# Kernel tuning notes

Hardware: AMD Instinct MI355X
Metric: run time of the kernel (lower is better)

Reference implementation:

```python
import jax, jax.numpy as jnp
import numpy as np

D = 128          # embedding_size
K = 1024         # num_embedding
DECAY = 0.99
EPS = 1e-5
VQ_COMMIT = 0.25
B, T = 16, 4096


def setup_inputs() -> dict:
    key = jax.random.key(0)
    k1, k2, k3 = jax.random.split(key, 3)
    emb = jax.random.normal(k2, (D, K), dtype=jnp.float32)
    return {
        "input": jax.random.normal(k1, (B, T, D), dtype=jnp.float32),
        "embedding": emb,
        "cluster_size": jnp.zeros((K,), dtype=jnp.float32),
        "embedding_mean": emb.copy(),
    }


def reference(input, embedding, cluster_size, embedding_mean):
    # ---- quantize: squared-distance argmin over codebook ----
    flatten = input.reshape(-1, D)                                   # [N, D]
    dist = ((flatten ** 2).sum(1, keepdims=True)
            - 2.0 * flatten @ embedding
            + (embedding ** 2).sum(0, keepdims=True))                # [N, K]
    embedding_ind = jnp.argmin(dist, axis=1)                         # [N]
    code = embedding_ind.reshape(input.shape[:-1])                   # [B, T]

    # ---- dequantize: codebook gather ----
    quantize = jnp.take(embedding.T, code, axis=0)                   # [B, T, D]

    # ---- EMA codebook update (training mode) ----
    N = flatten.shape[0]
    counts = jax.ops.segment_sum(jnp.ones((N,), input.dtype), embedding_ind,
                                 num_segments=K)                     # [K]
    emb_sum = jax.ops.segment_sum(flatten, embedding_ind,
                                  num_segments=K).T                  # [D, K]
    new_cluster_size = cluster_size * DECAY + (1.0 - DECAY) * counts
    new_embedding_mean = embedding_mean * DECAY + (1.0 - DECAY) * emb_sum
    n = new_cluster_size.sum()
    cs = (new_cluster_size + EPS) / (n + K * EPS) * n
    new_embedding = new_embedding_mean / cs[None, :]                 # [D, K]

    # ---- straight-through estimator + commitment loss ----
    quantize_st = input + jax.lax.stop_gradient(quantize - input)
    diff = VQ_COMMIT * jnp.mean(
        (jax.lax.stop_gradient(quantize_st) - input) ** 2)

    return (quantize_st, diff, code,
            new_embedding, new_cluster_size, new_embedding_mean)
```

## Files before the change

kernel.cpp:

```cpp
#include <hip/hip_runtime.h>
#include <hip/hip_fp16.h>
#include <math.h>

#define D_ 128
#define K_ 1024
#define N_ 65536
#define DECAY_ 0.99f
#define OMD_ 0.01f
#define EPS_ 1e-5f
#define VQC_ 0.25f
#define M1_ 0.14f
#define M2_ 0.14f
#define BIAS_ 96.0f
#define CLMIN_ 0.5f
#define CLMAX_ 508.0f
#define WSEG 32

typedef __attribute__((ext_vector_type(8))) _Float16 half8;
typedef __attribute__((ext_vector_type(4))) float f32x4;

#define WOFF_CODE  0
#define WOFF_E2    65536
#define WOFF_CNT   66560
#define WOFF_SSQ   67584
#define WOFF_RCNT  67585
#define WOFF_BASE  67648
#define WOFF_CURS  68736
#define WOFF_ORDER 69760
#define WOFF_ET    136320
#define WOFF_PART  267392
#define WOFF_CSORT 398464
#define WOFF_RLIST 791680
#define WOFF_EF    857216

#define OOFF_Q     0
#define OOFF_DIFF  8388608
#define OOFF_CODE  8388609
#define OOFF_NEMB  8454145
#define OOFF_NCS   8585217
#define OOFF_NMEAN 8586241

__device__ __forceinline__ unsigned umin32(unsigned a, unsigned b) { return a < b ? a : b; }
__device__ __forceinline__ unsigned umax32(unsigned a, unsigned b) { return a > b ? a : b; }

__device__ __forceinline__ void gld16(const unsigned short* g, unsigned short* l) {
    __builtin_amdgcn_global_load_lds(
        (const __attribute__((address_space(1))) unsigned int*)g,
        (__attribute__((address_space(3))) unsigned int*)l, 16, 0, 0);
}

__launch_bounds__(256)
__global__ void k_prep(const float* __restrict__ E, float* __restrict__ Et,
                       unsigned short* __restrict__ Ef, float* __restrict__ e2,
                       int* __restrict__ cnt, float* __restrict__ part1) {
    __shared__ float tile[128 * 17];
    __shared__ float e2s[16];
    int tid = threadIdx.x;
    int b = blockIdx.x;
    int c0 = b * 16;
    if (b == 0) {
        for (int i = tid; i < 1026; i += 256) cnt[i] = 0;
    }
    #pragma unroll
    for (int i = 0; i < 8; ++i) part1[b * 2048 + i * 256 + tid] = 0.f;
    if (tid < 16) e2s[tid] = 0.f;
    #pragma unroll
    for (int i = 0; i < 8; ++i) {
        int idx = i * 256 + tid;
        int d = idx >> 4, cc = idx & 15;
        tile[d * 17 + cc] = E[d * K_ + c0 + cc];
    }
    __syncthreads();
    #pragma unroll
    for (int i = 0; i < 8; ++i) {
        int idx = i * 256 + tid;
        int cc = idx >> 7, d = idx & 127;
        Et[(size_t)(c0 + cc) * D_ + d] = tile[d * 17 + cc];
    }
    int L = tid & 63, s = tid >> 6;
    int cc = L & 15;
    int d0 = s * 32 + ((L >> 4) << 3);
    unsigned short h[8];
    float sq = 0.f;
    #pragma unroll
    for (int j = 0; j < 8; ++j) {
        float e = tile[(d0 + j) * 17 + cc];
        sq = fmaf(e, e, sq);
        h[j] = __half_as_ushort(__float2half(-2.f * e));
    }
    int T = b * 256 + tid;
    #pragma unroll
    for (int j = 0; j < 8; ++j) Ef[T * 8 + j] = h[j];
    atomicAdd(&e2s[cc], sq);
    __syncthreads();
    if (tid < 16) e2[c0 + tid] = e2s[tid];
}

__launch_bounds__(512, 4)
__global__ void k_argmin_mfma(const float* __restrict__ x, const unsigned short* __restrict__ Ef,
                              const float* __restrict__ e2,
                              int* __restrict__ code_i, float* __restrict__ code_f,
                              int* __restrict__ cnt, int* __restrict__ rcnt,
                              int* __restrict__ rlist, const float* __restrict__ Et) {
    __shared__ unsigned short Bs[3][8192];
    __shared__ float e2s[K_];
    int tid = threadIdx.x;
    int w = tid >> 6, L = tid & 63, quad = L >> 4, col = L & 15;
    int mg = w >> 1, ng = w & 1;
    int n0 = blockIdx.x * 128;

    for (int i = tid; i < K_; i += 512) e2s[i] = e2[i];

    half8 ah[2][4];
    #pragma unroll
    for (int mt = 0; mt < 2; ++mt) {
        int tok = n0 + (2 * mg + mt) * 16 + col;
        #pragma unroll
        for (int s = 0; s < 4; ++s) {
            const float* p = x + (size_t)tok * D_ + s * 32 + quad * 8;
            float4 u0 = *(const float4*)(p);
            float4 u1 = *(const float4*)(p + 4);
            ah[mt][s][0] = (_Float16)u0.x; ah[mt][s][1] = (_Float16)u0.y;
            ah[mt][s][2] = (_Float16)u0.z; ah[mt][s][3] = (_Float16)u0.w;
            ah[mt][s][4] = (_Float16)u1.x; ah[mt][s][5] = (_Float16)u1.y;
            ah[mt][s][6] = (_Float16)u1.z; ah[mt][s][7] = (_Float16)u1.w;
        }
    }

    unsigned k1[2][4], k2[2][4], k3[2][4];
    #pragma unroll
    for (int mt = 0; mt < 2; ++mt)
        #pragma unroll
        for (int r = 0; r < 4; ++r) {
            k1[mt][r] = 0xFFFFFFFFu; k2[mt][r] = 0xFFFFFFFFu; k3[mt][r] = 0xFFFFFFFFu;
        }

    __syncthreads();

    #pragma unroll
    for (int i = 0; i < 2; ++i) {
        int o = (w * 2 + i) * 512;
        gld16(Ef + o + L * 8, &Bs[0][o]);
    }
    #pragma unroll
    for (int i = 0; i < 2; ++i) {
        int o = (w * 2 + i) * 512;
        gld16(Ef + 8192 + o + L * 8, &Bs[1][o]);
    }

    #pragma unroll
    for (int q = 0; q < 16; ++q) {
        if (q < 15) asm volatile("s_waitcnt vmcnt(2)" ::: "memory");
        else        asm volatile("s_waitcnt vmcnt(0)" ::: "memory");
        __builtin_amdgcn_s_barrier();
        asm volatile("" ::: "memory");

        const unsigned short* Bp = &Bs[q % 3][0];

        float evb[2];
        #pragma unroll
        for (int nn = 0; nn < 2; ++nn)
            evb[nn] = e2s[q * 64 + (2 * ng + nn) * 16 + col] + BIAS_;
        f32x4 acc[2][2];
        #pragma unroll
        for (int mt = 0; mt < 2; ++mt)
            #pragma unroll
            for (int nn = 0; nn < 2; ++nn)
                #pragma unroll
                for (int r = 0; r < 4; ++r)
                    acc[mt][nn][r] = evb[nn];

        #pragma unroll
        for (int s = 0; s < 4; ++s) {
            half8 bh[2];
            #pragma unroll
            for (int nn = 0; nn < 2; ++nn) {
                int off = (((2 * ng + nn) * 4 + s) * 64 + L) * 8;
                bh[nn] = *(const half8*)(Bp + off);
            }
            #pragma unroll
            for (int nn = 0; nn < 2; ++nn)
                #pragma unroll
                for (int mt = 0; mt < 2; ++mt)
                    acc[mt][nn] = __builtin_amdgcn_mfma_f32_16x16x32_f16(ah[mt][s], bh[nn], acc[mt][nn], 0, 0, 0);
        }

        #pragma unroll
        for (int nn = 0; nn < 2; ++nn) {
            unsigned cb = (unsigned)(q * 64 + (2 * ng + nn) * 16 + col);
            #pragma unroll
            for (int mt = 0; mt < 2; ++mt)
                #pragma unroll
                for (int r = 0; r < 4; ++r) {
                    float dc = fminf(fmaxf(acc[mt][nn][r], CLMIN_), CLMAX_);
                    unsigned key = (__float_as_uint(dc) & 0xFFFFFC00u) | cb;
                    unsigned m1 = umax32(k1[mt][r], key);
                    k1[mt][r]   = umin32(k1[mt][r], key);
                    unsigned m2 = umax32(k2[mt][r], m1);
                    k2[mt][r]   = umin32(k2[mt][r], m1);
                    k3[mt][r]   = umin32(k3[mt][r], m2);
                }
        }

        if (q < 14) {
            const unsigned short* src = Ef + (q + 2) * 8192;
            int sl = (q + 2) % 3;
            #pragma unroll
            for (int i = 0; i < 2; ++i) {
                int o = (w * 2 + i) * 512;
                gld16(src + o + L * 8, &Bs[sl][o]);
            }
        }
    }

    __syncthreads();
    unsigned* mk1 = (unsigned*)&Bs[0][0];
    unsigned* mk2 = mk1 + 256;
    unsigned* mk3 = mk2 + 256;

    #pragma unroll
    for (int mt = 0; mt < 2; ++mt) {
        #pragma unroll
        for (int r = 0; r < 4; ++r) {
            unsigned a = k1[mt][r], b = k2[mt][r], c = k3[mt][r];
            #pragma unroll
            for (int m = 1; m < 16; m <<= 1) {
                unsigned ao = (unsigned)__shfl_xor((int)a, m);
                unsigned bo = (unsigned)__shfl_xor((int)b, m);
                unsigned co = (unsigned)__shfl_xor((int)c, m);
                unsigned t1 = umax32(a, ao);
                a           = umin32(a, ao);
                unsigned s2 = umin32(b, bo);
                unsigned u  = umax32(t1, s2);
                b           = umin32(t1, s2);
                c           = umin32(u, umin32(c, co));
            }
            if (col == 0) {
                int tl = (2 * mg + mt) * 16 + quad * 4 + r;
                mk1[tl * 2 + ng] = a;
                mk2[tl * 2 + ng] = b;
                mk3[tl * 2 + ng] = c;
            }
        }
    }
    __syncthreads();
    if (tid < 128) {
        unsigned a1 = mk1[tid * 2], b1 = mk1[tid * 2 + 1];
        unsigned a2 = mk2[tid * 2], b2 = mk2[tid * 2 + 1];
        unsigned a3 = mk3[tid * 2], b3 = mk3[tid * 2 + 1];
        unsigned t1 = umax32(a1, b1);
        unsigned kk1 = umin32(a1, b1);
        unsigned s2 = umin32(a2, b2);
        unsigned kk2 = umin32(t1, s2);
        unsigned u  = umax32(t1, s2);
        unsigned kk3 = umin32(u, umin32(a3, b3));

        int i1 = (int)(kk1 & 1023u), i2 = (int)(kk2 & 1023u);
        float d1 = __uint_as_float(kk1 & 0xFFFFFC00u);
        float d2 = __uint_as_float(kk2 & 0xFFFFFC00u);
        float d3 = __uint_as_float(kk3 & 0xFFFFFC00u);
        int tok = n0 + tid;

        if (d3 - d1 < M2_) {
            code_i[tok] = i1;
            code_f[tok] = (float)i1;
            atomicAdd(cnt + i1, 1);
            int p = atomicAdd(rcnt, 1);
            rlist[p] = tok;
        } else {
            int win = i1;
            if (d2 - d1 < M1_) {
                const float* xr = x  + (size_t)tok * D_;
                const float* ea = Et + (size_t)i1 * D_;
                const float* eb = Et + (size_t)i2 * D_;
                float s1 = 0.f, sB = 0.f;
                #pragma unroll 4
                for (int dd = 0; dd < D_; dd += 4) {
                    float4 xv = *(const float4*)(xr + dd);
                    float4 av = *(const float4*)(ea + dd);
                    float4 bv = *(const float4*)(eb + dd);
                    s1 = fmaf(xv.x, av.x, s1); s1 = fmaf(xv.y, av.y, s1);
                    s1 = fmaf(xv.z, av.z, s1); s1 = fmaf(xv.w, av.w, s1);
                    sB = fmaf(xv.x, bv.x, sB); sB = fmaf(xv.y, bv.y, sB);
                    sB = fmaf(xv.z, bv.z, sB); sB = fmaf(xv.w, bv.w, sB);
                }
                float ex1 = e2s[i1] - 2.f * s1;
                float ex2 = e2s[i2] - 2.f * sB;
                if (ex2 < ex1 || (ex2 == ex1 && i2 < i1)) win = i2;
            }
            code_i[tok] = win;
            code_f[tok] = (float)win;
            atomicAdd(cnt + win, 1);
        }
    }
}

__launch_bounds__(256)
__global__ void k_fix(const float* __restrict__ x, const float* __restrict__ Et,
                      const float* __restrict__ e2, const int* __restrict__ rcnt,
                      const int* __restrict__ rlist, int* __restrict__ code_i,
                      float* __restrict__ code_f, int* __restrict__ cnt) {
    __shared__ float4 xs[32];
    __shared__ float sd[8];
    __shared__ int   si[8];
    int tid = threadIdx.x;
    int lane = tid & 63, w = tid >> 6;
    int half = lane >> 5;
    int q32  = lane & 31;
    int slot = w * 2 + half;
    int nr = *rcnt;
    for (int it = blockIdx.x; it < nr; it += gridDim.x) {
        __syncthreads();
        int tok = rlist[it];
        if (tid < 32) xs[tid] = ((const float4*)(x + (size_t)tok * D_))[tid];
        __syncthreads();
        float4 xv = xs[q32];
        float bd = INFINITY; int bb = 0;
        for (int c0 = 0; c0 < K_; c0 += 8) {
            int c = c0 + slot;
            float4 e = ((const float4*)(Et + (size_t)c * D_))[q32];
            float dot = xv.x * e.x + xv.y * e.y + xv.z * e.z + xv.w * e.w;
            dot += __shfl_xor(dot, 1);
            dot += __shfl_xor(dot, 2);
            dot += __shfl_xor(dot, 4);
            dot += __shfl_xor(dot, 8);
            dot += __shfl_xor(dot, 16);
            float dist = e2[c] - 2.f * dot;
            if (dist < bd) { bd = dist; bb = c; }
        }
        if (q32 == 0) { sd[slot] = bd; si[slot] = bb; }
        __syncthreads();
        if (tid == 0) {
            float fb = sd[0]; int fi = si[0];
            #pragma unroll
            for (int s = 1; s < 8; ++s) {
                if (sd[s] < fb || (sd[s] == fb && si[s] < fi)) { fb = sd[s]; fi = si[s]; }
            }
            int ob = code_i[tok];
            if (fi != ob) {
                code_i[tok] = fi;
                code_f[tok] = (float)fi;
                atomicAdd(cnt + ob, -1);
                atomicAdd(cnt + fi, 1);
            }
        }
    }
}

__launch_bounds__(256)
__global__ void k_scan(const int* __restrict__ cnt, int* __restrict__ base,
                       int* __restrict__ cursor) {
    int t = threadIdx.x;
    int lane = t & 63, wv = t >> 6;
    int c[4];
    #pragma unroll
    for (int j = 0; j < 4; ++j) c[j] = cnt[4 * t + j];
    int s = c[0] + c[1] + c[2] + c[3];
    int ps = s;
    #pragma unroll
    for (int m = 1; m < 64; m <<= 1) {
        int o = __shfl_up(ps, m);
        if (lane >= m) ps += o;
    }
    __shared__ int wtot[4];
    if (lane == 63) wtot[wv] = ps;
    __syncthreads();
    int woff = 0;
    for (int i = 0; i < 4; ++i) if (i < wv) woff += wtot[i];
    int run = woff + ps - s;
    #pragma unroll
    for (int j = 0; j < 4; ++j) {
        cursor[4 * t + j] = run;
        run += c[j];
        base[4 * t + j + 1] = run;
    }
    if (t == 0) base[0] = 0;
}

__global__ void k_scatter(const int* __restrict__ code_i, int* __restrict__ cursor,
                          int* __restrict__ order, int* __restrict__ csort) {
    int n = blockIdx.x * 256 + threadIdx.x;
    int c = code_i[n];
    int pos = atomicAdd(cursor + c, 1);
    order[pos] = n;
    csort[pos] = c;
}

__launch_bounds__(128)
__global__ void k_segdeq(const float* __restrict__ x, const float* __restrict__ Et,
                         const int* __restrict__ order, const int* __restrict__ csort,
                         float* __restrict__ part1, float* __restrict__ outq,
                         float* __restrict__ ssqp) {
    __shared__ int sn[WSEG], sc[WSEG];
    int d = threadIdx.x;
    int i0 = blockIdx.x * WSEG;
    if (d < WSEG) { sn[d] = order[i0 + d]; sc[d] = csort[i0 + d]; }
    __syncthreads();
    int cprev = sc[0];
    float eq = Et[(size_t)cprev * D_ + d];
    float acc = 0.f, ssql = 0.f;
    float xv = x[(size_t)sn[0] * D_ + d];
    #pragma unroll 4
    for (int j = 0; j < WSEG; ++j) {
        float xn = (j < WSEG - 1) ? x[(size_t)sn[j + 1] * D_ + d] : 0.f;
        int c = sc[j];
        if (c != cprev) {
            atomicAdd(&part1[(size_t)cprev * D_ + d], acc);
            acc = 0.f;
            eq = Et[(size_t)c * D_ + d];
            cprev = c;
        }
        float qv = xv + (eq - xv);
        outq[(size_t)sn[j] * D_ + d] = qv;
        float t = qv - xv;
        ssql = fmaf(t, t, ssql);
        acc += xv;
        xv = xn;
    }
    atomicAdd(&part1[(size_t)cprev * D_ + d], acc);

    #pragma unroll
    for (int off = 32; off > 0; off >>= 1) ssql += __shfl_down(ssql, off);
    __shared__ float wsum[2];
    if ((d & 63) == 0) wsum[d >> 6] = ssql;
    __syncthreads();
    if (d == 0) atomicAdd(ssqp, wsum[0] + wsum[1]);
}

__launch_bounds__(256)
__global__ void k_embed(const float* __restrict__ em, const float* __restrict__ part1,
                        const int* __restrict__ cnt, const float* __restrict__ csz,
                        const float* __restrict__ ssqp, float* __restrict__ out_nmean,
                        float* __restrict__ out_nemb, float* __restrict__ out_ncs,
                        float* __restrict__ out_diff) {
    int tid = threadIdx.x;
    __shared__ float red[256];

    float ls = 0.f;
    for (int j = tid; j < K_; j += 256) ls += csz[j] * DECAY_ + OMD_ * (float)cnt[j];
    red[tid] = ls;
    __syncthreads();
    for (int off = 128; off > 0; off >>= 1) {
        if (tid < off) red[tid] += red[tid + off];
        __syncthreads();
    }
    float n = red[0];
    __syncthreads();

    if (blockIdx.x == 0) {
        for (int j = tid; j < K_; j += 256)
            out_ncs[j] = csz[j] * DECAY_ + OMD_ * (float)cnt[j];
        if (tid == 0) *out_diff = VQC_ * ssqp[0] / (float)(N_ * D_);
    }

    int i = blockIdx.x * 256 + tid;
    int k = i & (K_ - 1);
    int d = i >> 10;
    float ncs_k = csz[k] * DECAY_ + OMD_ * (float)cnt[k];
    float csk = (ncs_k + EPS_) / (n + (float)K_ * EPS_) * n;
    float es = part1[(size_t)k * D_ + d];
    float nm = em[i] * DECAY_ + OMD_ * es;
    out_nmean[i] = nm;
    out_nemb[i]  = nm / csk;
}

extern "C" void kernel_launch(void* const* d_in, const int* in_sizes, int n_in,
                              void* d_out, int out_size, void* d_ws, size_t ws_size,
                              hipStream_t stream) {
    const float* x   = (const float*)d_in[0];
    const float* E   = (const float*)d_in[1];
    const float* csz = (const float*)d_in[2];
    const float* em  = (const float*)d_in[3];
    float* out = (float*)d_out;
    float* W   = (float*)d_ws;

    int*   code_i = (int*)(W + WOFF_CODE);
    float* e2     = W + WOFF_E2;
    int*   cnt    = (int*)(W + WOFF_CNT);
    float* ssqp   = W + WOFF_SSQ;
    int*   rcnt   = (int*)(W + WOFF_RCNT);
    int*   base   = (int*)(W + WOFF_BASE);
    int*   cursor = (int*)(W + WOFF_CURS);
    int*   order  = (int*)(W + WOFF_ORDER);
    float* Et     = W + WOFF_ET;
    float* part1  = W + WOFF_PART;
    int*   csort  = (int*)(W + WOFF_CSORT);
    int*   rlist  = (int*)(W + WOFF_RLIST);
    unsigned short* Ef = (unsigned short*)(W + WOFF_EF);

    k_prep<<<64, 256, 0, stream>>>(E, Et, Ef, e2, cnt, part1);
    k_argmin_mfma<<<N_ / 128, 512, 0, stream>>>(x, Ef, e2, code_i,
                                                out + OOFF_CODE, cnt, rcnt, rlist, Et);
    k_fix<<<1024, 256, 0, stream>>>(x, Et, e2, rcnt, rlist, code_i, out + OOFF_CODE, cnt);
    k_scan<<<1, 256, 0, stream>>>(cnt, base, cursor);
    k_scatter<<<N_ / 256, 256, 0, stream>>>(code_i, cursor, order, csort);
    k_segdeq<<<N_ / WSEG, 128, 0, stream>>>(x, Et, order, csort, part1,
                                            out + OOFF_Q, ssqp);
    k_embed<<<(D_ * K_) / 256, 256, 0, stream>>>(em, part1, cnt, csz, ssqp,
                                                 out + OOFF_NMEAN, out + OOFF_NEMB,
                                                 out + OOFF_NCS, out + OOFF_DIFF);
}
```

Before: 237.6 us.

## Split argmin codebook halves across blocks and move finalization to a separate kernel

```diff
diff --git a/kernel.cpp b/kernel.cpp
--- a/kernel.cpp
+++ b/kernel.cpp
@@ -32,6 +32,8 @@
 #define WOFF_CSORT 398464
 #define WOFF_RLIST 791680
 #define WOFF_EF    857216
+#define WOFF_KB    922752
+#define WOFF_E2H   1315968
 
 #define OOFF_Q     0
 #define OOFF_DIFF  8388608
@@ -52,7 +54,8 @@
 __launch_bounds__(256)
 __global__ void k_prep(const float* __restrict__ E, float* __restrict__ Et,
                        unsigned short* __restrict__ Ef, float* __restrict__ e2,
-                       int* __restrict__ cnt, float* __restrict__ part1) {
+                       float* __restrict__ e2h, int* __restrict__ cnt,
+                       float* __restrict__ part1) {
     __shared__ float tile[128 * 17];
     __shared__ float e2s[16];
     int tid = threadIdx.x;
@@ -93,59 +96,55 @@
     for (int j = 0; j < 8; ++j) Ef[T * 8 + j] = h[j];
     atomicAdd(&e2s[cc], sq);
     __syncthreads();
-    if (tid < 16) e2[c0 + tid] = e2s[tid];
-}
-
-__launch_bounds__(512, 4)
+    if (tid < 16) {
+        int c = c0 + tid;
+        e2[c] = e2s[tid];
+        e2h[((c >> 5) & 1) * 512 + (c >> 6) * 32 + (c & 31)] = e2s[tid];
+    }
+}
+
+__launch_bounds__(256, 6)
 __global__ void k_argmin_mfma(const float* __restrict__ x, const unsigned short* __restrict__ Ef,
-                              const float* __restrict__ e2,
-                              int* __restrict__ code_i, float* __restrict__ code_f,
-                              int* __restrict__ cnt, int* __restrict__ rcnt,
-                              int* __restrict__ rlist, const float* __restrict__ Et) {
-    __shared__ unsigned short Bs[3][8192];
-    __shared__ float e2s[K_];
+                              const float* __restrict__ e2h, unsigned* __restrict__ kb) {
+    __shared__ unsigned short Bs[3][4096];
+    __shared__ float e2s[512];
     int tid = threadIdx.x;
     int w = tid >> 6, L = tid & 63, quad = L >> 4, col = L & 15;
-    int mg = w >> 1, ng = w & 1;
-    int n0 = blockIdx.x * 128;
-
-    for (int i = tid; i < K_; i += 512) e2s[i] = e2[i];
-
-    half8 ah[2][4];
-    #pragma unroll
-    for (int mt = 0; mt < 2; ++mt) {
-        int tok = n0 + (2 * mg + mt) * 16 + col;
-        #pragma unroll
-        for (int s = 0; s < 4; ++s) {
-            const float* p = x + (size_t)tok * D_ + s * 32 + quad * 8;
-            float4 u0 = *(const float4*)(p);
-            float4 u1 = *(const float4*)(p + 4);
-            ah[mt][s][0] = (_Float16)u0.x; ah[mt][s][1] = (_Float16)u0.y;
-            ah[mt][s][2] = (_Float16)u0.z; ah[mt][s][3] = (_Float16)u0.w;
-            ah[mt][s][4] = (_Float16)u1.x; ah[mt][s][5] = (_Float16)u1.y;
-            ah[mt][s][6] = (_Float16)u1.z; ah[mt][s][7] = (_Float16)u1.w;
-        }
-    }
-
-    unsigned k1[2][4], k2[2][4], k3[2][4];
-    #pragma unroll
-    for (int mt = 0; mt < 2; ++mt)
-        #pragma unroll
-        for (int r = 0; r < 4; ++r) {
-            k1[mt][r] = 0xFFFFFFFFu; k2[mt][r] = 0xFFFFFFFFu; k3[mt][r] = 0xFFFFFFFFu;
-        }
+    int bx = blockIdx.x;
+    int ng = bx & 1;
+    int n0 = (bx >> 1) * 64;
+
+    e2s[tid]       = e2h[ng * 512 + tid];
+    e2s[tid + 256] = e2h[ng * 512 + tid + 256];
+
+    half8 ah[4];
+    int tok = n0 + w * 16 + col;
+    #pragma unroll
+    for (int s = 0; s < 4; ++s) {
+        const float* p = x + (size_t)tok * D_ + s * 32 + quad * 8;
+        float4 u0 = *(const float4*)(p);
+        float4 u1 = *(const float4*)(p + 4);
+        ah[s][0] = (_Float16)u0.x; ah[s][1] = (_Float16)u0.y;
+        ah[s][2] = (_Float16)u0.z; ah[s][3] = (_Float16)u0.w;
+        ah[s][4] = (_Float16)u1.x; ah[s][5] = (_Float16)u1.y;
+        ah[s][6] = (_Float16)u1.z; ah[s][7] = (_Float16)u1.w;
+    }
+
+    unsigned k1[4], k2[4], k3[4];
+    #pragma unroll
+    for (int r = 0; r < 4; ++r) { k1[r] = 0xFFFFFFFFu; k2[r] = 0xFFFFFFFFu; k3[r] = 0xFFFFFFFFu; }
 
     __syncthreads();
 
     #pragma unroll
     for (int i = 0; i < 2; ++i) {
         int o = (w * 2 + i) * 512;
-        gld16(Ef + o + L * 8, &Bs[0][o]);
+        gld16(Ef + ng * 4096 + o + L * 8, &Bs[0][o]);
     }
     #pragma unroll
     for (int i = 0; i < 2; ++i) {
         int o = (w * 2 + i) * 512;
-        gld16(Ef + 8192 + o + L * 8, &Bs[1][o]);
+        gld16(Ef + 8192 + ng * 4096 + o + L * 8, &Bs[1][o]);
     }
 
     #pragma unroll
@@ -157,53 +156,43 @@
 
         const unsigned short* Bp = &Bs[q % 3][0];
 
-        float evb[2];
+        f32x4 acc[2];
         #pragma unroll
-        for (int nn = 0; nn < 2; ++nn)
-            evb[nn] = e2s[q * 64 + (2 * ng + nn) * 16 + col] + BIAS_;
-        f32x4 acc[2][2];
-        #pragma unroll
-        for (int mt = 0; mt < 2; ++mt)
-            #pragma unroll
-            for (int nn = 0; nn < 2; ++nn)
-                #pragma unroll
-                for (int r = 0; r < 4; ++r)
-                    acc[mt][nn][r] = evb[nn];
+        for (int nn = 0; nn < 2; ++nn) {
+            float ev = e2s[q * 32 + nn * 16 + col] + BIAS_;
+            acc[nn] = (f32x4){ev, ev, ev, ev};
+        }
 
         #pragma unroll
         for (int s = 0; s < 4; ++s) {
             half8 bh[2];
             #pragma unroll
             for (int nn = 0; nn < 2; ++nn) {
-                int off = (((2 * ng + nn) * 4 + s) * 64 + L) * 8;
+                int off = ((nn * 4 + s) * 64 + L) * 8;
                 bh[nn] = *(const half8*)(Bp + off);
             }
             #pragma unroll
             for (int nn = 0; nn < 2; ++nn)
-                #pragma unroll
-                for (int mt = 0; mt < 2; ++mt)
-                    acc[mt][nn] = __builtin_amdgcn_mfma_f32_16x16x32_f16(ah[mt][s], bh[nn], acc[mt][nn], 0, 0, 0);
+                acc[nn] = __builtin_amdgcn_mfma_f32_16x16x32_f16(ah[s], bh[nn], acc[nn], 0, 0, 0);
         }
 
         #pragma unroll
         for (int nn = 0; nn < 2; ++nn) {
-            unsigned cb = (unsigned)(q * 64 + (2 * ng + nn) * 16 + col);
+            unsigned cb = (unsigned)(q * 64 + ng * 32 + nn * 16 + col);
             #pragma unroll
-            for (int mt = 0; mt < 2; ++mt)
-                #pragma unroll
-                for (int r = 0; r < 4; ++r) {
-                    float dc = fminf(fmaxf(acc[mt][nn][r], CLMIN_), CLMAX_);
-                    unsigned key = (__float_as_uint(dc) & 0xFFFFFC00u) | cb;
-                    unsigned m1 = umax32(k1[mt][r], key);
-                    k1[mt][r]   = umin32(k1[mt][r], key);
-                    unsigned m2 = umax32(k2[mt][r], m1);
-                    k2[mt][r]   = umin32(k2[mt][r], m1);
-                    k3[mt][r]   = umin32(k3[mt][r], m2);
-                }
+            for (int r = 0; r < 4; ++r) {
+                float dc = fminf(fmaxf(acc[nn][r], CLMIN_), CLMAX_);
+                unsigned key = (__float_as_uint(dc) & 0xFFFFFC00u) | cb;
+                unsigned m1 = umax32(k1[r], key);
+                k1[r]       = umin32(k1[r], key);
+                unsigned m2 = umax32(k2[r], m1);
+                k2[r]       = umin32(k2[r], m1);
+                k3[r]       = umin32(k3[r], m2);
+            }
         }
 
         if (q < 14) {
-            const unsigned short* src = Ef + (q + 2) * 8192;
+            const unsigned short* src = Ef + (q + 2) * 8192 + ng * 4096;
             int sl = (q + 2) % 3;
             #pragma unroll
             for (int i = 0; i < 2; ++i) {
@@ -213,85 +202,83 @@
         }
     }
 
-    __syncthreads();
-    unsigned* mk1 = (unsigned*)&Bs[0][0];
-    unsigned* mk2 = mk1 + 256;
-    unsigned* mk3 = mk2 + 256;
-
-    #pragma unroll
-    for (int mt = 0; mt < 2; ++mt) {
+    #pragma unroll
+    for (int r = 0; r < 4; ++r) {
+        unsigned a = k1[r], b = k2[r], c = k3[r];
         #pragma unroll
-        for (int r = 0; r < 4; ++r) {
-            unsigned a = k1[mt][r], b = k2[mt][r], c = k3[mt][r];
-            #pragma unroll
-            for (int m = 1; m < 16; m <<= 1) {
-                unsigned ao = (unsigned)__shfl_xor((int)a, m);
-                unsigned bo = (unsigned)__shfl_xor((int)b, m);
-                unsigned co = (unsigned)__shfl_xor((int)c, m);
-                unsigned t1 = umax32(a, ao);
-                a           = umin32(a, ao);
-                unsigned s2 = umin32(b, bo);
-                unsigned u  = umax32(t1, s2);
-                b           = umin32(t1, s2);
-                c           = umin32(u, umin32(c, co));
-            }
-            if (col == 0) {
-                int tl = (2 * mg + mt) * 16 + quad * 4 + r;
-                mk1[tl * 2 + ng] = a;
-                mk2[tl * 2 + ng] = b;
-                mk3[tl * 2 + ng] = c;
-            }
-        }
-    }
-    __syncthreads();
-    if (tid < 128) {
-        unsigned a1 = mk1[tid * 2], b1 = mk1[tid * 2 + 1];
-        unsigned a2 = mk2[tid * 2], b2 = mk2[tid * 2 + 1];
-        unsigned a3 = mk3[tid * 2], b3 = mk3[tid * 2 + 1];
-        unsigned t1 = umax32(a1, b1);
-        unsigned kk1 = umin32(a1, b1);
-        unsigned s2 = umin32(a2, b2);
-        unsigned kk2 = umin32(t1, s2);
-        unsigned u  = umax32(t1, s2);
-        unsigned kk3 = umin32(u, umin32(a3, b3));
-
-        int i1 = (int)(kk1 & 1023u), i2 = (int)(kk2 & 1023u);
-        float d1 = __uint_as_float(kk1 & 0xFFFFFC00u);
-        float d2 = __uint_as_float(kk2 & 0xFFFFFC00u);
-        float d3 = __uint_as_float(kk3 & 0xFFFFFC00u);
-        int tok = n0 + tid;
-
-        if (d3 - d1 < M2_) {
-            code_i[tok] = i1;
-            code_f[tok] = (float)i1;
-            atomicAdd(cnt + i1, 1);
-            int p = atomicAdd(rcnt, 1);
-            rlist[p] = tok;
-        } else {
-            int win = i1;
-            if (d2 - d1 < M1_) {
-                const float* xr = x  + (size_t)tok * D_;
-                const float* ea = Et + (size_t)i1 * D_;
-                const float* eb = Et + (size_t)i2 * D_;
-                float s1 = 0.f, sB = 0.f;
-                #pragma unroll 4
-                for (int dd = 0; dd < D_; dd += 4) {
-                    float4 xv = *(const float4*)(xr + dd);
-                    float4 av = *(const float4*)(ea + dd);
-                    float4 bv = *(const float4*)(eb + dd);
-                    s1 = fmaf(xv.x, av.x, s1); s1 = fmaf(xv.y, av.y, s1);
-                    s1 = fmaf(xv.z, av.z, s1); s1 = fmaf(xv.w, av.w, s1);
-                    sB = fmaf(xv.x, bv.x, sB); sB = fmaf(xv.y, bv.y, sB);
-                    sB = fmaf(xv.z, bv.z, sB); sB = fmaf(xv.w, bv.w, sB);
-                }
-                float ex1 = e2s[i1] - 2.f * s1;
-                float ex2 = e2s[i2] - 2.f * sB;
-                if (ex2 < ex1 || (ex2 == ex1 && i2 < i1)) win = i2;
-            }
-            code_i[tok] = win;
-            code_f[tok] = (float)win;
-            atomicAdd(cnt + win, 1);
-        }
+        for (int m = 1; m < 16; m <<= 1) {
+            unsigned ao = (unsigned)__shfl_xor((int)a, m);
+            unsigned bo = (unsigned)__shfl_xor((int)b, m);
+            unsigned co = (unsigned)__shfl_xor((int)c, m);
+            unsigned t1 = umax32(a, ao);
+            a           = umin32(a, ao);
+            unsigned s2 = umin32(b, bo);
+            unsigned u  = umax32(t1, s2);
+            b           = umin32(t1, s2);
+            c           = umin32(u, umin32(c, co));
+        }
+        if (col == 0) {
+            int gt = n0 + w * 16 + quad * 4 + r;
+            unsigned base = (unsigned)gt * 6u + (unsigned)ng * 3u;
+            kb[base]     = a;
+            kb[base + 1] = b;
+            kb[base + 2] = c;
+        }
+    }
+}
+
+__launch_bounds__(256)
+__global__ void k_post(const float* __restrict__ x, const float* __restrict__ Et,
+                       const float* __restrict__ e2, const unsigned* __restrict__ kb,
+                       int* __restrict__ code_i, float* __restrict__ code_f,
+                       int* __restrict__ cnt, int* __restrict__ rcnt,
+                       int* __restrict__ rlist) {
+    int tid = threadIdx.x;
+    int lane = tid & 63;
+    int tok = blockIdx.x * 256 + tid;
+    const uint2* kp = (const uint2*)(kb + (size_t)tok * 6);
+    uint2 v0 = kp[0], v1 = kp[1], v2 = kp[2];
+    unsigned a1 = v0.x, a2 = v0.y, a3 = v1.x;
+    unsigned b1 = v1.y, b2 = v2.x, b3 = v2.y;
+    unsigned t1 = umax32(a1, b1), kk1 = umin32(a1, b1);
+    unsigned s2 = umin32(a2, b2), kk2 = umin32(t1, s2);
+    unsigned u  = umax32(t1, s2), kk3 = umin32(u, umin32(a3, b3));
+    int i1 = (int)(kk1 & 1023u), i2 = (int)(kk2 & 1023u);
+    float d1 = __uint_as_float(kk1 & 0xFFFFFC00u);
+    float d2 = __uint_as_float(kk2 & 0xFFFFFC00u);
+    float d3 = __uint_as_float(kk3 & 0xFFFFFC00u);
+    bool trip  = (d3 - d1 < M2_);
+    bool needp = !trip && (d2 - d1 < M1_);
+    int win = i1;
+
+    unsigned long long mask = __ballot(needp);
+    while (mask) {
+        int src = (int)(__ffsll((unsigned long long)mask)) - 1;
+        mask &= mask - 1;
+        int tt = __shfl(tok, src);
+        int j1 = __shfl(i1, src), j2 = __shfl(i2, src);
+        int q32 = lane & 31, hf = lane >> 5;
+        float4 xv = ((const float4*)(x + (size_t)tt * D_))[q32];
+        float4 ev = ((const float4*)(Et + (size_t)(hf ? j2 : j1) * D_))[q32];
+        float dot = xv.x * ev.x + xv.y * ev.y + xv.z * ev.z + xv.w * ev.w;
+        dot += __shfl_xor(dot, 1);
+        dot += __shfl_xor(dot, 2);
+        dot += __shfl_xor(dot, 4);
+        dot += __shfl_xor(dot, 8);
+        dot += __shfl_xor(dot, 16);
+        float dA = __shfl(dot, 0), dB = __shfl(dot, 32);
+        float ex1 = e2[j1] - 2.f * dA;
+        float ex2 = e2[j2] - 2.f * dB;
+        int wn = (ex2 < ex1 || (ex2 == ex1 && j2 < j1)) ? j2 : j1;
+        if (lane == src) win = wn;
+    }
+
+    code_i[tok] = win;
+    code_f[tok] = (float)win;
+    atomicAdd(cnt + win, 1);
+    if (trip) {
+        int p = atomicAdd(rcnt, 1);
+        rlist[p] = tok;
     }
 }
 
@@ -487,10 +474,13 @@
     int*   csort  = (int*)(W + WOFF_CSORT);
     int*   rlist  = (int*)(W + WOFF_RLIST);
     unsigned short* Ef = (unsigned short*)(W + WOFF_EF);
-
-    k_prep<<<64, 256, 0, stream>>>(E, Et, Ef, e2, cnt, part1);
-    k_argmin_mfma<<<N_ / 128, 512, 0, stream>>>(x, Ef, e2, code_i,
-                                                out + OOFF_CODE, cnt, rcnt, rlist, Et);
+    unsigned* kb  = (unsigned*)(W + WOFF_KB);
+    float* e2h    = W + WOFF_E2H;
+
+    k_prep<<<64, 256, 0, stream>>>(E, Et, Ef, e2, e2h, cnt, part1);
+    k_argmin_mfma<<<(N_ / 64) * 2, 256, 0, stream>>>(x, Ef, e2h, kb);
+    k_post<<<N_ / 256, 256, 0, stream>>>(x, Et, e2, kb, code_i, out + OOFF_CODE,
+                                         cnt, rcnt, rlist);
     k_fix<<<1024, 256, 0, stream>>>(x, Et, e2, rcnt, rlist, code_i, out + OOFF_CODE, cnt);
     k_scan<<<1, 256, 0, stream>>>(cnt, base, cursor);
     k_scatter<<<N_ / 256, 256, 0, stream>>>(code_i, cursor, order, csort);
```

Measured after the change: 345.1 us. 1.45x slower.
